# Optimization experiments

Hardware: AMD Instinct MI355X
Metric: run time of the kernel (lower is better)

Reference implementation:

```python
import jax, jax.numpy as jnp
import numpy as np

# Constants derived from quantiles=[0.1..0.9] (deciles), df = 9.
QUANTILES = jnp.array([0.1, 0.2, 0.3, 0.4, 0.5, 0.6, 0.7, 0.8, 0.9], dtype=jnp.float32)
# scipy.stats.norm.ppf(quantiles), cast to float32 as in the torch module
Z_SCORES = jnp.array([-1.2815516, -0.8416212, -0.5244005, -0.2533471, 0.0,
                      0.2533471, 0.5244005, 0.8416212, 1.2815516], dtype=jnp.float32)
# expected bin probabilities: q0, diffs, 1-q_last -> all 0.1 for deciles
EXPECTED_PCT = jnp.full((10,), 0.1, dtype=jnp.float32)
# chi2.ppf(1 - p, df=9) for p in QUANTILES (precomputed with scipy offline)
CRIT = jnp.array([14.683657, 12.242145, 10.656372, 9.413640, 8.342832,
                  7.357034, 6.393306, 5.380053, 4.168159], dtype=jnp.float32)
MAX_CRIT = 14.683657
SHARPNESS = 100.0  # sigmoid steepness for the soft histogram


def setup_inputs() -> dict:
    key = jax.random.key(0)
    x = jax.random.normal(key, (16777216,), dtype=jnp.float32)
    return {"x": x}


def reference(x):
    n = x.shape[0]
    mean = x.mean()
    std = jnp.std(x, ddof=1)  # torch.std uses Bessel's correction
    z = (x - mean) / std  # [n]
    # soft cumulative counts at each quantile threshold: [K]
    cum = jax.nn.sigmoid(SHARPNESS * (Z_SCORES[:, None] - z[None, :])).sum(axis=1)
    # bin counts: first cum, consecutive diffs, remainder n - last cum -> [K+1]
    actual = jnp.concatenate([cum[:1], jnp.diff(cum),
                              jnp.asarray(n, z.dtype)[None] - cum[-1:]])
    expected = n * EXPECTED_PCT
    chi2_stat = jnp.sum((actual - expected) ** 2 / (expected + 1e-7))
    # differentiable interpolation of p-value
    w = jax.nn.softmax(-jnp.abs(chi2_stat - CRIT))
    p_value_estimate = 1.0 - jnp.sum(w * QUANTILES)
    excess = jax.nn.relu((chi2_stat - MAX_CRIT) / 100.0)
    return p_value_estimate + excess
```

## Files before the change

kernel.cpp:

```cpp
#include <hip/hip_runtime.h>
#include <math.h>


#if __has_builtin(__builtin_amdgcn_exp2f)
#define EXP2F(x) __builtin_amdgcn_exp2f(x)
#else
#define EXP2F(x) exp2f(x)
#endif
#if __has_builtin(__builtin_amdgcn_rcpf)
#define RCPF(x) __builtin_amdgcn_rcpf(x)
#else
#define RCPF(x) (1.0f / (x))
#endif

#define NBLK 1024

static __device__ __forceinline__ double wave_reduce_d(double v) {
#pragma unroll
    for (int off = 32; off > 0; off >>= 1) v += __shfl_down(v, off);
    return v;
}

__global__ __launch_bounds__(256) void pass1_stats(const float* __restrict__ x,
                                                   double* __restrict__ part1, int n) {
    const int tx = threadIdx.x;
    const int tid = blockIdx.x * 256 + tx;
    const int nthreads = NBLK * 256;
    const int n4 = n >> 2;
    const float4* __restrict__ x4 = (const float4*)x;

    float fs = 0.f, fss = 0.f;
    for (int i = tid; i < n4; i += nthreads) {
        float4 v = x4[i];
        fs += (v.x + v.y) + (v.z + v.w);
        fss = fmaf(v.x, v.x, fss); fss = fmaf(v.y, v.y, fss);
        fss = fmaf(v.z, v.z, fss); fss = fmaf(v.w, v.w, fss);
    }
    if (blockIdx.x == 0 && tx == 0) {
        for (int j = n4 << 2; j < n; ++j) {
            float v = x[j];
            fs += v;
            fss = fmaf(v, v, fss);
        }
    }

    double s = wave_reduce_d((double)fs);
    double ss = wave_reduce_d((double)fss);
    __shared__ double sm[4][2];
    const int lane = tx & 63, wid = tx >> 6;
    if (lane == 0) { sm[wid][0] = s; sm[wid][1] = ss; }
    __syncthreads();
    if (tx == 0) {
        double ts = (sm[0][0] + sm[1][0]) + (sm[2][0] + sm[3][0]);
        double tss = (sm[0][1] + sm[1][1]) + (sm[2][1] + sm[3][1]);
        part1[2 * blockIdx.x] = ts;
        part1[2 * blockIdx.x + 1] = tss;
    }
}

__global__ __launch_bounds__(256) void reduce_stats(const double* __restrict__ part1,
                                                    float* __restrict__ sb, int n) {
    const int tx = threadIdx.x;
    double s = 0.0, ss = 0.0;
    for (int b = tx; b < NBLK; b += 256) {
        s += part1[2 * b];
        ss += part1[2 * b + 1];
    }
    double rs = wave_reduce_d(s);
    double rss = wave_reduce_d(ss);
    __shared__ double sm[4][2];
    const int lane = tx & 63, wid = tx >> 6;
    if (lane == 0) { sm[wid][0] = rs; sm[wid][1] = rss; }
    __syncthreads();
    if (tx == 0) {
        double ts = (sm[0][0] + sm[1][0]) + (sm[2][0] + sm[3][0]);
        double tss = (sm[0][1] + sm[1][1]) + (sm[2][1] + sm[3][1]);
        const double Ld = 144.26950408889634;
        const double nd = (double)n;
        const double mean = ts / nd;
        const double var = (tss - ts * ts / nd) / (nd - 1.0);
        const double inv_std = 1.0 / sqrt(var);
        sb[0] = (float)(Ld * inv_std);
        sb[1] = (float)(-Ld * inv_std * mean);
    }
}

__global__ __launch_bounds__(256) void pass2_cum(const float* __restrict__ x,
                                                 const float* __restrict__ sb,
                                                 double* __restrict__ part2, int n) {
    constexpr float C0 = -184.888834f, C1 = -121.420293f, C2 = -75.655000f,
                    C3 = -36.550261f, C4 = 0.0f, C5 = 36.550261f,
                    C6 = 75.655000f, C7 = 121.420293f, C8 = 184.888834f;
    const float S = sb[0], B = sb[1];

    float acc[9];
#pragma unroll
    for (int k = 0; k < 9; ++k) acc[k] = 0.f;

    auto process = [&](float xv) {
        const float a = fmaf(xv, S, B);
        acc[0] += RCPF(1.0f + EXP2F(a - C0));
        acc[1] += RCPF(1.0f + EXP2F(a - C1));
        acc[2] += RCPF(1.0f + EXP2F(a - C2));
        acc[3] += RCPF(1.0f + EXP2F(a - C3));
        acc[4] += RCPF(1.0f + EXP2F(a - C4));
        acc[5] += RCPF(1.0f + EXP2F(a - C5));
        acc[6] += RCPF(1.0f + EXP2F(a - C6));
        acc[7] += RCPF(1.0f + EXP2F(a - C7));
        acc[8] += RCPF(1.0f + EXP2F(a - C8));
    };

    const int tx = threadIdx.x;
    const int tid = blockIdx.x * 256 + tx;
    const int nthreads = NBLK * 256;
    const int n4 = n >> 2;
    const float4* __restrict__ x4 = (const float4*)x;

    for (int i = tid; i < n4; i += nthreads) {
        float4 v = x4[i];
        process(v.x); process(v.y); process(v.z); process(v.w);
    }
    if (blockIdx.x == 0 && tx == 0) {
        for (int jj = n4 << 2; jj < n; ++jj) process(x[jj]);
    }

    __shared__ double sm[4][9];
    const int lane = tx & 63, wid = tx >> 6;
#pragma unroll
    for (int k = 0; k < 9; ++k) {
        double r = wave_reduce_d((double)acc[k]);
        if (lane == 0) sm[wid][k] = r;
    }
    __syncthreads();
    if (tx < 9) {
        double t = (sm[0][tx] + sm[1][tx]) + (sm[2][tx] + sm[3][tx]);
        part2[9 * blockIdx.x + tx] = t;
    }
}

__global__ __launch_bounds__(256) void finalize_kernel(const double* __restrict__ part2,
                                                       float* __restrict__ out, int n) {
    const int tx = threadIdx.x;
    double acc[9];
#pragma unroll
    for (int k = 0; k < 9; ++k) acc[k] = 0.0;
    for (int b = tx; b < NBLK; b += 256) {
#pragma unroll
        for (int k = 0; k < 9; ++k) acc[k] += part2[9 * b + k];
    }
    __shared__ double sm[4][9];
    const int lane = tx & 63, wid = tx >> 6;
#pragma unroll
    for (int k = 0; k < 9; ++k) {
        double r = wave_reduce_d(acc[k]);
        if (lane == 0) sm[wid][k] = r;
    }
    __syncthreads();
    if (tx == 0) {
        const double CRIT[9] = {14.683657, 12.242145, 10.656372, 9.413640, 8.342832,
                                7.357034,  6.393306,  5.380053,  4.168159};
        const double nd = (double)n;
        double cum[9];
#pragma unroll
        for (int k = 0; k < 9; ++k)
            cum[k] = (sm[0][k] + sm[1][k]) + (sm[2][k] + sm[3][k]);

        double actual[10];
        actual[0] = cum[0];
#pragma unroll
        for (int k = 1; k < 9; ++k) actual[k] = cum[k] - cum[k - 1];
        actual[9] = nd - cum[8];

        const double expected = nd * (double)0.1f;
        const double denom = expected + 1e-7;
        double chi2 = 0.0;
#pragma unroll
        for (int j = 0; j < 10; ++j) {
            double d = actual[j] - expected;
            chi2 += d * d / denom;
        }

        double dneg[9], m = -1e300;
#pragma unroll
        for (int k = 0; k < 9; ++k) {
            dneg[k] = -fabs(chi2 - CRIT[k]);
            if (dneg[k] > m) m = dneg[k];
        }
        double W = 0.0, PQ = 0.0;
#pragma unroll
        for (int k = 0; k < 9; ++k) {
            double w = exp(dneg[k] - m);
            W += w;
            PQ += w * (0.1 * (double)(k + 1));
        }
        double p = 1.0 - PQ / W;
        double excess = (chi2 - 14.683657) / 100.0;
        if (excess < 0.0) excess = 0.0;
        out[0] = (float)(p + excess);
    }
}

extern "C" void kernel_launch(void* const* d_in, const int* in_sizes, int n_in,
                              void* d_out, int out_size, void* d_ws, size_t ws_size,
                              hipStream_t stream) {
    const float* x = (const float*)d_in[0];
    const int n = in_sizes[0];

    double* part1 = (double*)d_ws;
    double* part2 = part1 + 2 * NBLK;
    float* sb = (float*)(part2 + 9 * NBLK);

    pass1_stats<<<NBLK, 256, 0, stream>>>(x, part1, n);
    reduce_stats<<<1, 256, 0, stream>>>(part1, sb, n);
    pass2_cum<<<NBLK, 256, 0, stream>>>(x, sb, part2, n);
    finalize_kernel<<<1, 256, 0, stream>>>(part2, (float*)d_out, n);
}
```

Before: 130.3 us.

## Fuse four kernel launches into one cooperative kernel with grid syncs

Replaces the stats, reduce, sigmoid-sum and finalize launches with a single cooperative kernel that uses grid.sync between phases. Every block redundantly reduces the per-block partial sums to get mean and std, and block 0 computes the final chi-square result. The goal is to remove the launch gaps and tail effects of the two single-block kernels. It costs two grid-wide barriers, makes the grid size depend on an occupancy query, and keeps the old multi-kernel path as a fallback if the cooperative launch fails.

```diff
diff --git a/kernel.cpp b/kernel.cpp
--- a/kernel.cpp
+++ b/kernel.cpp
@@ -1,5 +1,8 @@
 #include <hip/hip_runtime.h>
+#include <hip/hip_cooperative_groups.h>
 #include <math.h>
+
+namespace cg = cooperative_groups;
 
 
 #if __has_builtin(__builtin_amdgcn_exp2f)
@@ -13,7 +16,8 @@
 #define RCPF(x) (1.0f / (x))
 #endif
 
-#define NBLK 1024
+#define MAXBLK 1024
+#define NCU 256
 
 static __device__ __forceinline__ double wave_reduce_d(double v) {
 #pragma unroll
@@ -21,11 +25,190 @@
     return v;
 }
 
+__device__ __forceinline__ float sig9_a(float a, float* acc) {
+    constexpr float C0 = -184.888834f, C1 = -121.420293f, C2 = -75.655000f,
+                    C3 = -36.550261f, C4 = 0.0f, C5 = 36.550261f,
+                    C6 = 75.655000f, C7 = 121.420293f, C8 = 184.888834f;
+    acc[0] += RCPF(1.0f + EXP2F(a - C0));
+    acc[1] += RCPF(1.0f + EXP2F(a - C1));
+    acc[2] += RCPF(1.0f + EXP2F(a - C2));
+    acc[3] += RCPF(1.0f + EXP2F(a - C3));
+    acc[4] += RCPF(1.0f + EXP2F(a - C4));
+    acc[5] += RCPF(1.0f + EXP2F(a - C5));
+    acc[6] += RCPF(1.0f + EXP2F(a - C6));
+    acc[7] += RCPF(1.0f + EXP2F(a - C7));
+    acc[8] += RCPF(1.0f + EXP2F(a - C8));
+    return a;
+}
+
+__device__ void epilogue(const double* cum, float* out, int n) {
+    const double CRIT[9] = {14.683657, 12.242145, 10.656372, 9.413640, 8.342832,
+                            7.357034,  6.393306,  5.380053,  4.168159};
+    const double nd = (double)n;
+    double actual[10];
+    actual[0] = cum[0];
+#pragma unroll
+    for (int k = 1; k < 9; ++k) actual[k] = cum[k] - cum[k - 1];
+    actual[9] = nd - cum[8];
+    const double expected = nd * (double)0.1f;
+    const double denom = expected + 1e-7;
+    double chi2 = 0.0;
+#pragma unroll
+    for (int j = 0; j < 10; ++j) {
+        double d = actual[j] - expected;
+        chi2 += d * d / denom;
+    }
+    double dneg[9], m = -1e300;
+#pragma unroll
+    for (int k = 0; k < 9; ++k) {
+        dneg[k] = -fabs(chi2 - CRIT[k]);
+        if (dneg[k] > m) m = dneg[k];
+    }
+    double W = 0.0, PQ = 0.0;
+#pragma unroll
+    for (int k = 0; k < 9; ++k) {
+        double w = exp(dneg[k] - m);
+        W += w;
+        PQ += w * (0.1 * (double)(k + 1));
+    }
+    double p = 1.0 - PQ / W;
+    double excess = (chi2 - 14.683657) / 100.0;
+    if (excess < 0.0) excess = 0.0;
+    out[0] = (float)(p + excess);
+}
+
+__global__ __launch_bounds__(256, 4) void fused_kernel(const float* __restrict__ x,
+                                                       double* __restrict__ ws,
+                                                       float* __restrict__ out, int n) {
+    cg::grid_group grid = cg::this_grid();
+    double* __restrict__ part1 = ws;
+    double* __restrict__ part2 = ws + 2 * MAXBLK;
+
+    const int tx = threadIdx.x;
+    const int bid = blockIdx.x;
+    const int nblk = gridDim.x;
+    const int tid = bid * 256 + tx;
+    const int nthreads = nblk * 256;
+    const int n4 = n >> 2;
+    const float4* __restrict__ x4 = (const float4*)x;
+    const int lane = tx & 63, wid = tx >> 6;
+
+    __shared__ double sm[4][9];
+    __shared__ float sSB[2];
+
+    {
+        float fs = 0.f, fss = 0.f;
+        for (int i = tid; i < n4; i += nthreads) {
+            float4 v = x4[i];
+            fs += (v.x + v.y) + (v.z + v.w);
+            fss = fmaf(v.x, v.x, fss); fss = fmaf(v.y, v.y, fss);
+            fss = fmaf(v.z, v.z, fss); fss = fmaf(v.w, v.w, fss);
+        }
+        if (bid == 0 && tx == 0) {
+            for (int j = n4 << 2; j < n; ++j) {
+                float v = x[j];
+                fs += v;
+                fss = fmaf(v, v, fss);
+            }
+        }
+        double s = wave_reduce_d((double)fs);
+        double ss = wave_reduce_d((double)fss);
+        if (lane == 0) { sm[wid][0] = s; sm[wid][1] = ss; }
+        __syncthreads();
+        if (tx == 0) {
+            part1[2 * bid] = (sm[0][0] + sm[1][0]) + (sm[2][0] + sm[3][0]);
+            part1[2 * bid + 1] = (sm[0][1] + sm[1][1]) + (sm[2][1] + sm[3][1]);
+        }
+        __syncthreads();
+    }
+
+    grid.sync();
+
+    {
+        double s = 0.0, ss = 0.0;
+        for (int b = tx; b < nblk; b += 256) {
+            s += part1[2 * b];
+            ss += part1[2 * b + 1];
+        }
+        double rs = wave_reduce_d(s);
+        double rss = wave_reduce_d(ss);
+        if (lane == 0) { sm[wid][0] = rs; sm[wid][1] = rss; }
+        __syncthreads();
+        if (tx == 0) {
+            double ts = (sm[0][0] + sm[1][0]) + (sm[2][0] + sm[3][0]);
+            double tss = (sm[0][1] + sm[1][1]) + (sm[2][1] + sm[3][1]);
+            const double Ld = 144.26950408889634;
+            const double nd = (double)n;
+            const double mean = ts / nd;
+            const double var = (tss - ts * ts / nd) / (nd - 1.0);
+            const double inv_std = 1.0 / sqrt(var);
+            sSB[0] = (float)(Ld * inv_std);
+            sSB[1] = (float)(-Ld * inv_std * mean);
+        }
+        __syncthreads();
+    }
+    const float S = sSB[0], B = sSB[1];
+
+    {
+        float acc[9];
+#pragma unroll
+        for (int k = 0; k < 9; ++k) acc[k] = 0.f;
+
+        for (int i = tid; i < n4; i += nthreads) {
+            float4 v = x4[i];
+            sig9_a(fmaf(v.x, S, B), acc);
+            sig9_a(fmaf(v.y, S, B), acc);
+            sig9_a(fmaf(v.z, S, B), acc);
+            sig9_a(fmaf(v.w, S, B), acc);
+        }
+        if (bid == 0 && tx == 0) {
+            for (int jj = n4 << 2; jj < n; ++jj) sig9_a(fmaf(x[jj], S, B), acc);
+        }
+
+        __syncthreads();
+#pragma unroll
+        for (int k = 0; k < 9; ++k) {
+            double r = wave_reduce_d((double)acc[k]);
+            if (lane == 0) sm[wid][k] = r;
+        }
+        __syncthreads();
+        if (tx < 9) {
+            part2[9 * bid + tx] = (sm[0][tx] + sm[1][tx]) + (sm[2][tx] + sm[3][tx]);
+        }
+    }
+
+    grid.sync();
+
+    if (bid == 0) {
+        double acc[9];
+#pragma unroll
+        for (int k = 0; k < 9; ++k) acc[k] = 0.0;
+        for (int b = tx; b < nblk; b += 256) {
+#pragma unroll
+            for (int k = 0; k < 9; ++k) acc[k] += part2[9 * b + k];
+        }
+        __syncthreads();
+#pragma unroll
+        for (int k = 0; k < 9; ++k) {
+            double r = wave_reduce_d(acc[k]);
+            if (lane == 0) sm[wid][k] = r;
+        }
+        __syncthreads();
+        if (tx == 0) {
+            double cum[9];
+#pragma unroll
+            for (int k = 0; k < 9; ++k)
+                cum[k] = (sm[0][k] + sm[1][k]) + (sm[2][k] + sm[3][k]);
+            epilogue(cum, out, n);
+        }
+    }
+}
+
 __global__ __launch_bounds__(256) void pass1_stats(const float* __restrict__ x,
                                                    double* __restrict__ part1, int n) {
     const int tx = threadIdx.x;
     const int tid = blockIdx.x * 256 + tx;
-    const int nthreads = NBLK * 256;
+    const int nthreads = gridDim.x * 256;
     const int n4 = n >> 2;
     const float4* __restrict__ x4 = (const float4*)x;
 
@@ -43,7 +226,6 @@
             fss = fmaf(v, v, fss);
         }
     }
-
     double s = wave_reduce_d((double)fs);
     double ss = wave_reduce_d((double)fss);
     __shared__ double sm[4][2];
@@ -51,10 +233,8 @@
     if (lane == 0) { sm[wid][0] = s; sm[wid][1] = ss; }
     __syncthreads();
     if (tx == 0) {
-        double ts = (sm[0][0] + sm[1][0]) + (sm[2][0] + sm[3][0]);
-        double tss = (sm[0][1] + sm[1][1]) + (sm[2][1] + sm[3][1]);
-        part1[2 * blockIdx.x] = ts;
-        part1[2 * blockIdx.x + 1] = tss;
+        part1[2 * blockIdx.x] = (sm[0][0] + sm[1][0]) + (sm[2][0] + sm[3][0]);
+        part1[2 * blockIdx.x + 1] = (sm[0][1] + sm[1][1]) + (sm[2][1] + sm[3][1]);
     }
 }
 
@@ -62,7 +242,7 @@
                                                     float* __restrict__ sb, int n) {
     const int tx = threadIdx.x;
     double s = 0.0, ss = 0.0;
-    for (int b = tx; b < NBLK; b += 256) {
+    for (int b = tx; b < MAXBLK; b += 256) {
         s += part1[2 * b];
         ss += part1[2 * b + 1];
     }
@@ -88,40 +268,26 @@
 __global__ __launch_bounds__(256) void pass2_cum(const float* __restrict__ x,
                                                  const float* __restrict__ sb,
                                                  double* __restrict__ part2, int n) {
-    constexpr float C0 = -184.888834f, C1 = -121.420293f, C2 = -75.655000f,
-                    C3 = -36.550261f, C4 = 0.0f, C5 = 36.550261f,
-                    C6 = 75.655000f, C7 = 121.420293f, C8 = 184.888834f;
     const float S = sb[0], B = sb[1];
-
     float acc[9];
 #pragma unroll
     for (int k = 0; k < 9; ++k) acc[k] = 0.f;
 
-    auto process = [&](float xv) {
-        const float a = fmaf(xv, S, B);
-        acc[0] += RCPF(1.0f + EXP2F(a - C0));
-        acc[1] += RCPF(1.0f + EXP2F(a - C1));
-        acc[2] += RCPF(1.0f + EXP2F(a - C2));
-        acc[3] += RCPF(1.0f + EXP2F(a - C3));
-        acc[4] += RCPF(1.0f + EXP2F(a - C4));
-        acc[5] += RCPF(1.0f + EXP2F(a - C5));
-        acc[6] += RCPF(1.0f + EXP2F(a - C6));
-        acc[7] += RCPF(1.0f + EXP2F(a - C7));
-        acc[8] += RCPF(1.0f + EXP2F(a - C8));
-    };
-
     const int tx = threadIdx.x;
     const int tid = blockIdx.x * 256 + tx;
-    const int nthreads = NBLK * 256;
+    const int nthreads = gridDim.x * 256;
     const int n4 = n >> 2;
     const float4* __restrict__ x4 = (const float4*)x;
 
     for (int i = tid; i < n4; i += nthreads) {
         float4 v = x4[i];
-        process(v.x); process(v.y); process(v.z); process(v.w);
+        sig9_a(fmaf(v.x, S, B), acc);
+        sig9_a(fmaf(v.y, S, B), acc);
+        sig9_a(fmaf(v.z, S, B), acc);
+        sig9_a(fmaf(v.w, S, B), acc);
     }
     if (blockIdx.x == 0 && tx == 0) {
-        for (int jj = n4 << 2; jj < n; ++jj) process(x[jj]);
+        for (int jj = n4 << 2; jj < n; ++jj) sig9_a(fmaf(x[jj], S, B), acc);
     }
 
     __shared__ double sm[4][9];
@@ -133,8 +299,7 @@
     }
     __syncthreads();
     if (tx < 9) {
-        double t = (sm[0][tx] + sm[1][tx]) + (sm[2][tx] + sm[3][tx]);
-        part2[9 * blockIdx.x + tx] = t;
+        part2[9 * blockIdx.x + tx] = (sm[0][tx] + sm[1][tx]) + (sm[2][tx] + sm[3][tx]);
     }
 }
 
@@ -144,7 +309,7 @@
     double acc[9];
 #pragma unroll
     for (int k = 0; k < 9; ++k) acc[k] = 0.0;
-    for (int b = tx; b < NBLK; b += 256) {
+    for (int b = tx; b < MAXBLK; b += 256) {
 #pragma unroll
         for (int k = 0; k < 9; ++k) acc[k] += part2[9 * b + k];
     }
@@ -157,46 +322,11 @@
     }
     __syncthreads();
     if (tx == 0) {
-        const double CRIT[9] = {14.683657, 12.242145, 10.656372, 9.413640, 8.342832,
-                                7.357034,  6.393306,  5.380053,  4.168159};
-        const double nd = (double)n;
         double cum[9];
 #pragma unroll
         for (int k = 0; k < 9; ++k)
             cum[k] = (sm[0][k] + sm[1][k]) + (sm[2][k] + sm[3][k]);
-
-        double actual[10];
-        actual[0] = cum[0];
-#pragma unroll
-        for (int k = 1; k < 9; ++k) actual[k] = cum[k] - cum[k - 1];
-        actual[9] = nd - cum[8];
-
-        const double expected = nd * (double)0.1f;
-        const double denom = expected + 1e-7;
-        double chi2 = 0.0;
-#pragma unroll
-        for (int j = 0; j < 10; ++j) {
-            double d = actual[j] - expected;
-            chi2 += d * d / denom;
-        }
-
-        double dneg[9], m = -1e300;
-#pragma unroll
-        for (int k = 0; k < 9; ++k) {
-            dneg[k] = -fabs(chi2 - CRIT[k]);
-            if (dneg[k] > m) m = dneg[k];
-        }
-        double W = 0.0, PQ = 0.0;
-#pragma unroll
-        for (int k = 0; k < 9; ++k) {
-            double w = exp(dneg[k] - m);
-            W += w;
-            PQ += w * (0.1 * (double)(k + 1));
-        }
-        double p = 1.0 - PQ / W;
-        double excess = (chi2 - 14.683657) / 100.0;
-        if (excess < 0.0) excess = 0.0;
-        out[0] = (float)(p + excess);
+        epilogue(cum, out, n);
     }
 }
 
@@ -204,14 +334,27 @@
                               void* d_out, int out_size, void* d_ws, size_t ws_size,
                               hipStream_t stream) {
     const float* x = (const float*)d_in[0];
-    const int n = in_sizes[0];
-
-    double* part1 = (double*)d_ws;
-    double* part2 = part1 + 2 * NBLK;
-    float* sb = (float*)(part2 + 9 * NBLK);
-
-    pass1_stats<<<NBLK, 256, 0, stream>>>(x, part1, n);
+    int n = in_sizes[0];
+    double* ws = (double*)d_ws;
+    float* out = (float*)d_out;
+
+    int per_cu = 0;
+    hipError_t qerr = hipOccupancyMaxActiveBlocksPerMultiprocessor(
+        &per_cu, (const void*)fused_kernel, 256, 0);
+    if (qerr == hipSuccess && per_cu > 0) {
+        int nblk = per_cu * NCU;
+        if (nblk > MAXBLK) nblk = MAXBLK;
+        void* args[] = {(void*)&x, (void*)&ws, (void*)&out, (void*)&n};
+        hipError_t lerr = hipLaunchCooperativeKernel(
+            (const void*)fused_kernel, dim3(nblk), dim3(256), args, 0, stream);
+        if (lerr == hipSuccess) return;
+    }
+
+    double* part1 = ws;
+    double* part2 = ws + 2 * MAXBLK;
+    float* sb = (float*)(part2 + 9 * MAXBLK);
+    pass1_stats<<<MAXBLK, 256, 0, stream>>>(x, part1, n);
     reduce_stats<<<1, 256, 0, stream>>>(part1, sb, n);
-    pass2_cum<<<NBLK, 256, 0, stream>>>(x, sb, part2, n);
-    finalize_kernel<<<1, 256, 0, stream>>>(part2, (float*)d_out, n);
-}
+    pass2_cum<<<MAXBLK, 256, 0, stream>>>(x, sb, part2, n);
+    finalize_kernel<<<1, 256, 0, stream>>>(part2, out, n);
+}
```

After: 247.1 us. +89.6%, slower.

## Share one exp2 across sigmoid thresholds and fold stats reduction into pass2

Applied to the files above, without the earlier changes.

The sigmoid inner loop now computes a single exp2 of a half-scaled argument per element and builds each of the nine threshold terms as (E*g_k)^2 with precomputed per-threshold factors. This replaces nine transcendental evaluations per element with one plus a few multiplies. The separate single-block stats reduction kernel is removed, and every pass2 block instead redundantly reduces the 1024 partial sums, saving one launch. The risk is float overflow or underflow of E for outliers, which the squared form makes more extreme; saturated terms still resolve to 0 or 1 through the reciprocal.

```diff
diff --git a/kernel.cpp b/kernel.cpp
--- a/kernel.cpp
+++ b/kernel.cpp
@@ -21,6 +21,46 @@
     return v;
 }
 
+__device__ __constant__ double d_ZS[9] = {
+    -1.2815516, -0.8416212, -0.5244005, -0.2533471, 0.0,
+    0.2533471,  0.5244005,  0.8416212,  1.2815516};
+
+__device__ void epilogue(const double* cum, float* out, int n) {
+    const double CRIT[9] = {14.683657, 12.242145, 10.656372, 9.413640, 8.342832,
+                            7.357034,  6.393306,  5.380053,  4.168159};
+    const double nd = (double)n;
+    double actual[10];
+    actual[0] = cum[0];
+#pragma unroll
+    for (int k = 1; k < 9; ++k) actual[k] = cum[k] - cum[k - 1];
+    actual[9] = nd - cum[8];
+    const double expected = nd * (double)0.1f;
+    const double denom = expected + 1e-7;
+    double chi2 = 0.0;
+#pragma unroll
+    for (int j = 0; j < 10; ++j) {
+        double d = actual[j] - expected;
+        chi2 += d * d / denom;
+    }
+    double dneg[9], m = -1e300;
+#pragma unroll
+    for (int k = 0; k < 9; ++k) {
+        dneg[k] = -fabs(chi2 - CRIT[k]);
+        if (dneg[k] > m) m = dneg[k];
+    }
+    double W = 0.0, PQ = 0.0;
+#pragma unroll
+    for (int k = 0; k < 9; ++k) {
+        double w = exp(dneg[k] - m);
+        W += w;
+        PQ += w * (0.1 * (double)(k + 1));
+    }
+    double p = 1.0 - PQ / W;
+    double excess = (chi2 - 14.683657) / 100.0;
+    if (excess < 0.0) excess = 0.0;
+    out[0] = (float)(p + excess);
+}
+
 __global__ __launch_bounds__(256) void pass1_stats(const float* __restrict__ x,
                                                    double* __restrict__ part1, int n) {
     const int tx = threadIdx.x;
@@ -43,7 +83,6 @@
             fss = fmaf(v, v, fss);
         }
     }
-
     double s = wave_reduce_d((double)fs);
     double ss = wave_reduce_d((double)fss);
     __shared__ double sm[4][2];
@@ -51,66 +90,63 @@
     if (lane == 0) { sm[wid][0] = s; sm[wid][1] = ss; }
     __syncthreads();
     if (tx == 0) {
-        double ts = (sm[0][0] + sm[1][0]) + (sm[2][0] + sm[3][0]);
-        double tss = (sm[0][1] + sm[1][1]) + (sm[2][1] + sm[3][1]);
-        part1[2 * blockIdx.x] = ts;
-        part1[2 * blockIdx.x + 1] = tss;
-    }
-}
-
-__global__ __launch_bounds__(256) void reduce_stats(const double* __restrict__ part1,
-                                                    float* __restrict__ sb, int n) {
+        part1[2 * blockIdx.x] = (sm[0][0] + sm[1][0]) + (sm[2][0] + sm[3][0]);
+        part1[2 * blockIdx.x + 1] = (sm[0][1] + sm[1][1]) + (sm[2][1] + sm[3][1]);
+    }
+}
+
+__global__ __launch_bounds__(256) void pass2_cum(const float* __restrict__ x,
+                                                 const double* __restrict__ part1,
+                                                 double* __restrict__ part2, int n) {
     const int tx = threadIdx.x;
-    double s = 0.0, ss = 0.0;
-    for (int b = tx; b < NBLK; b += 256) {
-        s += part1[2 * b];
-        ss += part1[2 * b + 1];
-    }
-    double rs = wave_reduce_d(s);
-    double rss = wave_reduce_d(ss);
-    __shared__ double sm[4][2];
     const int lane = tx & 63, wid = tx >> 6;
-    if (lane == 0) { sm[wid][0] = rs; sm[wid][1] = rss; }
-    __syncthreads();
-    if (tx == 0) {
-        double ts = (sm[0][0] + sm[1][0]) + (sm[2][0] + sm[3][0]);
-        double tss = (sm[0][1] + sm[1][1]) + (sm[2][1] + sm[3][1]);
-        const double Ld = 144.26950408889634;
-        const double nd = (double)n;
-        const double mean = ts / nd;
-        const double var = (tss - ts * ts / nd) / (nd - 1.0);
-        const double inv_std = 1.0 / sqrt(var);
-        sb[0] = (float)(Ld * inv_std);
-        sb[1] = (float)(-Ld * inv_std * mean);
-    }
-}
-
-__global__ __launch_bounds__(256) void pass2_cum(const float* __restrict__ x,
-                                                 const float* __restrict__ sb,
-                                                 double* __restrict__ part2, int n) {
-    constexpr float C0 = -184.888834f, C1 = -121.420293f, C2 = -75.655000f,
-                    C3 = -36.550261f, C4 = 0.0f, C5 = 36.550261f,
-                    C6 = 75.655000f, C7 = 121.420293f, C8 = 184.888834f;
-    const float S = sb[0], B = sb[1];
+
+    __shared__ double sm[4][9];
+    __shared__ float sConst[11];
+    {
+        double s = 0.0, ss = 0.0;
+        for (int b = tx; b < NBLK; b += 256) {
+            s += part1[2 * b];
+            ss += part1[2 * b + 1];
+        }
+        double rs = wave_reduce_d(s);
+        double rss = wave_reduce_d(ss);
+        if (lane == 0) { sm[wid][0] = rs; sm[wid][1] = rss; }
+        __syncthreads();
+        if (tx == 0) {
+            double ts = (sm[0][0] + sm[1][0]) + (sm[2][0] + sm[3][0]);
+            double tss = (sm[0][1] + sm[1][1]) + (sm[2][1] + sm[3][1]);
+            const double Ld = 144.26950408889634;
+            const double nd = (double)n;
+            const double mean = ts / nd;
+            const double var = (tss - ts * ts / nd) / (nd - 1.0);
+            const double inv_std = 1.0 / sqrt(var);
+            sConst[0] = (float)(0.5 * Ld * inv_std);
+            sConst[1] = (float)(-0.5 * Ld * inv_std * mean);
+#pragma unroll
+            for (int k = 0; k < 9; ++k)
+                sConst[2 + k] = (float)exp2(-0.5 * Ld * d_ZS[k]);
+        }
+        __syncthreads();
+    }
+    const float S2 = sConst[0], B2 = sConst[1];
+    float sg[9];
+#pragma unroll
+    for (int k = 0; k < 9; ++k) sg[k] = sConst[2 + k];
 
     float acc[9];
 #pragma unroll
     for (int k = 0; k < 9; ++k) acc[k] = 0.f;
 
     auto process = [&](float xv) {
-        const float a = fmaf(xv, S, B);
-        acc[0] += RCPF(1.0f + EXP2F(a - C0));
-        acc[1] += RCPF(1.0f + EXP2F(a - C1));
-        acc[2] += RCPF(1.0f + EXP2F(a - C2));
-        acc[3] += RCPF(1.0f + EXP2F(a - C3));
-        acc[4] += RCPF(1.0f + EXP2F(a - C4));
-        acc[5] += RCPF(1.0f + EXP2F(a - C5));
-        acc[6] += RCPF(1.0f + EXP2F(a - C6));
-        acc[7] += RCPF(1.0f + EXP2F(a - C7));
-        acc[8] += RCPF(1.0f + EXP2F(a - C8));
+        const float E = EXP2F(fmaf(xv, S2, B2));
+#pragma unroll
+        for (int k = 0; k < 9; ++k) {
+            const float t = E * sg[k];
+            acc[k] += RCPF(1.0f + t * t);
+        }
     };
 
-    const int tx = threadIdx.x;
     const int tid = blockIdx.x * 256 + tx;
     const int nthreads = NBLK * 256;
     const int n4 = n >> 2;
@@ -124,8 +160,7 @@
         for (int jj = n4 << 2; jj < n; ++jj) process(x[jj]);
     }
 
-    __shared__ double sm[4][9];
-    const int lane = tx & 63, wid = tx >> 6;
+    __syncthreads();
 #pragma unroll
     for (int k = 0; k < 9; ++k) {
         double r = wave_reduce_d((double)acc[k]);
@@ -133,8 +168,7 @@
     }
     __syncthreads();
     if (tx < 9) {
-        double t = (sm[0][tx] + sm[1][tx]) + (sm[2][tx] + sm[3][tx]);
-        part2[9 * blockIdx.x + tx] = t;
+        part2[9 * blockIdx.x + tx] = (sm[0][tx] + sm[1][tx]) + (sm[2][tx] + sm[3][tx]);
     }
 }
 
@@ -157,46 +191,11 @@
     }
     __syncthreads();
     if (tx == 0) {
-        const double CRIT[9] = {14.683657, 12.242145, 10.656372, 9.413640, 8.342832,
-                                7.357034,  6.393306,  5.380053,  4.168159};
-        const double nd = (double)n;
         double cum[9];
 #pragma unroll
         for (int k = 0; k < 9; ++k)
             cum[k] = (sm[0][k] + sm[1][k]) + (sm[2][k] + sm[3][k]);
-
-        double actual[10];
-        actual[0] = cum[0];
-#pragma unroll
-        for (int k = 1; k < 9; ++k) actual[k] = cum[k] - cum[k - 1];
-        actual[9] = nd - cum[8];
-
-        const double expected = nd * (double)0.1f;
-        const double denom = expected + 1e-7;
-        double chi2 = 0.0;
-#pragma unroll
-        for (int j = 0; j < 10; ++j) {
-            double d = actual[j] - expected;
-            chi2 += d * d / denom;
-        }
-
-        double dneg[9], m = -1e300;
-#pragma unroll
-        for (int k = 0; k < 9; ++k) {
-            dneg[k] = -fabs(chi2 - CRIT[k]);
-            if (dneg[k] > m) m = dneg[k];
-        }
-        double W = 0.0, PQ = 0.0;
-#pragma unroll
-        for (int k = 0; k < 9; ++k) {
-            double w = exp(dneg[k] - m);
-            W += w;
-            PQ += w * (0.1 * (double)(k + 1));
-        }
-        double p = 1.0 - PQ / W;
-        double excess = (chi2 - 14.683657) / 100.0;
-        if (excess < 0.0) excess = 0.0;
-        out[0] = (float)(p + excess);
+        epilogue(cum, out, n);
     }
 }
 
@@ -205,13 +204,10 @@
                               hipStream_t stream) {
     const float* x = (const float*)d_in[0];
     const int n = in_sizes[0];
-
     double* part1 = (double*)d_ws;
     double* part2 = part1 + 2 * NBLK;
-    float* sb = (float*)(part2 + 9 * NBLK);
 
     pass1_stats<<<NBLK, 256, 0, stream>>>(x, part1, n);
-    reduce_stats<<<1, 256, 0, stream>>>(part1, sb, n);
-    pass2_cum<<<NBLK, 256, 0, stream>>>(x, sb, part2, n);
+    pass2_cum<<<NBLK, 256, 0, stream>>>(x, part1, part2, n);
     finalize_kernel<<<1, 256, 0, stream>>>(part2, (float*)d_out, n);
 }
```

New measurement: 125.0 us. -4.1%, faster.
